# Kernel tuning notes

Measured on AMD Instinct MI355X. Metric: run time of the kernel, lower is better.

## Reference

```python
import jax, jax.numpy as jnp
import numpy as np

B, D_IN, D_OUT = 8192, 4096, 4096
IN_DIMS = (64, 64)
OUT_DIMS = (64, 64)
# tt_rank_rate=0.5 over dims [64,64,64,64] -> ranks [1,32,1024,32,1]
RANKS = (1, 32, 1024, 32, 1)


def _kaiming_uniform(key, shape):
    # matches nn.init.kaiming_uniform_(a=sqrt(5)) on a (r_prev, d, r) tensor:
    # fan_in = prod(shape[1:]) = d * r, gain = sqrt(2/(1+5)) = sqrt(1/3)
    fan_in = shape[1] * shape[2]
    bound = np.sqrt(1.0 / 3.0) * np.sqrt(3.0 / fan_in)
    return jax.random.uniform(key, shape, jnp.float32, -bound, bound)


def setup_inputs() -> dict:
    key = jax.random.key(0)
    kx, k0, k1, k2, k3, kb = jax.random.split(key, 6)
    dims = list(IN_DIMS) + list(OUT_DIMS)
    shapes = [(RANKS[i], dims[i], RANKS[i + 1]) for i in range(4)]
    x = jax.random.normal(kx, (B, D_IN), jnp.float32)
    core0 = _kaiming_uniform(k0, shapes[0])  # (1, 64, 32)
    core1 = _kaiming_uniform(k1, shapes[1])  # (32, 64, 1024)
    core2 = _kaiming_uniform(k2, shapes[2])  # (1024, 64, 32)
    core3 = _kaiming_uniform(k3, shapes[3])  # (32, 64, 1)
    bb = 1.0 / np.sqrt(D_IN)
    bias = jax.random.uniform(kb, (D_OUT,), jnp.float32, -bb, bb)
    return {"x": x, "core0": core0, "core1": core1, "core2": core2,
            "core3": core3, "bias": bias}


def reference(x, core0, core1, core2, core3, bias):
    b = x.shape[0]
    s = x.reshape(b, IN_DIMS[0], IN_DIMS[1])          # (B, 64, 64)
    # input core 0: contract first input dim (rank-in = 1 squeezed)
    s = jnp.einsum('bcd,cs->bds', s, core0[0])        # (B, 64, 32)
    # input core 1: contract second input dim and rank
    s = jnp.einsum('bcr,rcs->bs', s, core1)           # (B, 1024)
    # output core 2: expand first output dim
    s = jnp.einsum('br,rAs->bAs', s, core2)           # (B, 64, 32)
    # output core 3: expand second output dim (rank-out = 1 squeezed)
    s = jnp.einsum('bAr,rB->bAB', s, core3[..., 0])   # (B, 64, 64)
    return s.reshape(b, -1) + bias                    # (B, 4096)
```

## Files before the change

kernel.cpp:

```cpp
#include <hip/hip_runtime.h>
#include <hip/hip_bf16.h>


typedef _Float16 h4 __attribute__((ext_vector_type(4)));
typedef _Float16 h8 __attribute__((ext_vector_type(8)));
typedef float f32x4 __attribute__((ext_vector_type(4)));

#define BATCH 8192

__device__ __forceinline__ void gld_lds16(const void* g, void* l) {
  __builtin_amdgcn_global_load_lds(
      (__attribute__((address_space(1))) void*)(g),
      (__attribute__((address_space(3))) void*)(l), 16, 0, 0);
}

__global__ __launch_bounds__(256) void transpose_cast2(
    const float* __restrict__ c1, _Float16* __restrict__ W1t,
    const float* __restrict__ c2, _Float16* __restrict__ W2t) {
  __shared__ float t[64][65];
  const int which = blockIdx.z;
  const float* src = which ? c2 : c1;
  _Float16* dst = which ? W2t : W1t;
  const int K = which ? 1024 : 2048, U = which ? 2048 : 1024;
  const int k0 = (which ? blockIdx.y : blockIdx.x) * 64;
  const int u0 = (which ? blockIdx.x : blockIdx.y) * 64;
  const int tx = threadIdx.x & 63, ty = threadIdx.x >> 6;
  for (int i = ty; i < 64; i += 4) {
    const int k = k0 + i;
    const int sr = which ? k : ((k & 31) * 64 + (k >> 5));
    t[i][tx] = src[(size_t)sr * U + u0 + tx];
  }
  __syncthreads();
  for (int i = ty; i < 64; i += 4) {
    dst[(size_t)(u0 + i) * K + k0 + tx] = (_Float16)t[tx][i];
  }
}

__global__ __launch_bounds__(256) void stage2(const float* __restrict__ x,
                                              const float* __restrict__ c0,
                                              _Float16* __restrict__ s1) {
  __shared__ _Float16 xh[4 * 4096];
  __shared__ float c0l[2048];
  const int b0 = blockIdx.x * 4;
  const int tid = threadIdx.x;

  {
    const float4* xg = (const float4*)(x + (size_t)b0 * 4096);
#pragma unroll
    for (int k = 0; k < 16; ++k) {
      float4 v = xg[tid + 256 * k];
      h4 w = {(_Float16)v.x, (_Float16)v.y, (_Float16)v.z, (_Float16)v.w};
      ((h4*)xh)[tid + 256 * k] = w;
    }
    ((float4*)c0l)[tid] = ((const float4*)c0)[tid];
    ((float4*)c0l)[tid + 256] = ((const float4*)c0)[tid + 256];
  }
  __syncthreads();

  const int row = tid >> 6, t6 = tid & 63;
  const int d0 = (t6 >> 3) * 8;
  const int r0 = (t6 & 7) * 4;
  const _Float16* xrow = xh + row * 4096;

  float acc[8][4];
#pragma unroll
  for (int i = 0; i < 8; ++i)
#pragma unroll
    for (int j = 0; j < 4; ++j) acc[i][j] = 0.0f;

  for (int c = 0; c < 64; ++c) {
    h8 xv = *(const h8*)&xrow[c * 64 + d0];
    f32x4 wv = *(const f32x4*)&c0l[c * 32 + r0];
#pragma unroll
    for (int i = 0; i < 8; ++i) {
      const float xf = (float)xv[i];
#pragma unroll
      for (int j = 0; j < 4; ++j) acc[i][j] += xf * wv[j];
    }
  }

  _Float16* s1row = s1 + (size_t)(b0 + row) * 2048;
#pragma unroll
  for (int i = 0; i < 8; ++i) {
    h4 o = {(_Float16)acc[i][0], (_Float16)acc[i][1], (_Float16)acc[i][2],
            (_Float16)acc[i][3]};
    *(h4*)&s1row[(d0 + i) * 32 + r0] = o;
  }
}

template <int K, int CN, bool FUSED>
__global__ __launch_bounds__(512, 2) void gemm_pipe(
    const _Float16* __restrict__ A, const _Float16* __restrict__ Bt,
    _Float16* __restrict__ C, const float* __restrict__ c3,
    const float* __restrict__ bias, float* __restrict__ out) {
  __shared__ __align__(16) char lds[3 * 49152];
  constexpr int NT = K / 64;
  const int bm = blockIdx.x, bn = blockIdx.y;
  const int tid = threadIdx.x;
  const int w = tid >> 6, lane = tid & 63;
  const int lr = lane & 15, kh = lane >> 4;
  const int wmo = (w >> 2) << 6, wno = (w & 3) << 6;

  f32x4 acc[4][4] = {};

  const int sr = tid >> 3;
  const int sc = ((tid & 7) ^ (sr & 7)) << 4;
  const char* gA = (const char*)(A + (size_t)(bm * 128 + sr) * K) + sc;
  const char* gB = (const char*)(Bt + (size_t)(bn * 256 + sr) * K) + sc;
  const size_t rk = (size_t)K * 128;
  char* lw = lds + (w << 10);

  auto STAGE = [&](int t) {
    char* b_ = lw + (t % 3) * 49152;
    const char* ga = gA + (size_t)t * 128;
    const char* gb = gB + (size_t)t * 128;
    gld_lds16(ga, b_);
    gld_lds16(ga + rk, b_ + 8192);
    gld_lds16(gb, b_ + 16384);
    gld_lds16(gb + rk, b_ + 24576);
    gld_lds16(gb + 2 * rk, b_ + 32768);
    gld_lds16(gb + 3 * rk, b_ + 40960);
  };

  auto KSTEP = [&](int t) {
    const char* bufA = lds + (t % 3) * 49152;
    const char* bufB = bufA + 16384;
    h8 af[2][4], bf[2][4];
#pragma unroll
    for (int kk = 0; kk < 2; ++kk) {
#pragma unroll
      for (int m = 0; m < 4; ++m) {
        const int R = wmo + m * 16 + lr;
        af[kk][m] = *(const h8*)(bufA + R * 128 +
                                 ((((kk << 2) + kh) ^ (R & 7)) << 4));
      }
#pragma unroll
      for (int n = 0; n < 4; ++n) {
        const int R = wno + n * 16 + lr;
        bf[kk][n] = *(const h8*)(bufB + R * 128 +
                                 ((((kk << 2) + kh) ^ (R & 7)) << 4));
      }
    }
    asm volatile("s_waitcnt lgkmcnt(0)" ::: "memory");
    __builtin_amdgcn_sched_barrier(0);
    __builtin_amdgcn_s_setprio(1);
#pragma unroll
    for (int kk = 0; kk < 2; ++kk)
#pragma unroll
      for (int m = 0; m < 4; ++m)
#pragma unroll
        for (int n = 0; n < 4; ++n)
          acc[m][n] = __builtin_amdgcn_mfma_f32_16x16x32_f16(
              af[kk][m], bf[kk][n], acc[m][n], 0, 0, 0);
    __builtin_amdgcn_s_setprio(0);
    __builtin_amdgcn_sched_barrier(0);
  };

  STAGE(0);
  STAGE(1);
  for (int t = 0; t < NT - 1; ++t) {
    asm volatile("s_waitcnt vmcnt(6)" ::: "memory");
    __builtin_amdgcn_s_barrier();
    __builtin_amdgcn_sched_barrier(0);
    if (t < NT - 2) STAGE(t + 2);
    KSTEP(t);
  }
  asm volatile("s_waitcnt vmcnt(0)" ::: "memory");
  __builtin_amdgcn_s_barrier();
  __builtin_amdgcn_sched_barrier(0);
  KSTEP(NT - 1);

  if constexpr (!FUSED) {
#pragma unroll
    for (int m = 0; m < 4; ++m) {
      const int r0 = bm * 128 + wmo + m * 16 + kh * 4;
#pragma unroll
      for (int n = 0; n < 4; ++n) {
        const int c0 = bn * 256 + wno + n * 16 + lr;
#pragma unroll
        for (int q = 0; q < 4; ++q)
          C[(size_t)(r0 + q) * CN + c0] = (_Float16)acc[m][n][q];
      }
    }
  } else {
    h8 bfe[4];
    float bb[8][4];
#pragma unroll
    for (int n = 0; n < 4; ++n) {
#pragma unroll
      for (int j = 0; j < 8; ++j)
        bfe[n][j] = (_Float16)c3[(kh * 8 + j) * 64 + n * 16 + lr];
#pragma unroll
      for (int a = 0; a < 8; ++a)
        bb[a][n] = bias[(bn * 8 + a) * 64 + n * 16 + lr];
    }
    __syncthreads();
#pragma unroll
    for (int m = 0; m < 4; ++m) {
      const int Rb = wmo + m * 16 + kh * 4;
#pragma unroll
      for (int n = 0; n < 4; ++n) {
        const int cc = wno + n * 16 + lr;
#pragma unroll
        for (int q = 0; q < 4; ++q) {
          const int R = Rb + q;
          *(_Float16*)(lds + R * 512 +
                       ((((cc >> 3) ^ (R & 7)) << 4) | ((cc & 7) << 1))) =
              (_Float16)acc[m][n][q];
        }
      }
    }
    __syncthreads();
    const int row = (w << 4) + lr;
    const int orow0 = bm * 128 + (w << 4) + (kh << 2);
#pragma unroll
    for (int a = 0; a < 8; ++a) {
      h8 afv = *(const h8*)(lds + row * 512 +
                            ((((a << 2) + kh) ^ (row & 7)) << 4));
#pragma unroll
      for (int n = 0; n < 4; ++n) {
        f32x4 d = {};
        d = __builtin_amdgcn_mfma_f32_16x16x32_f16(afv, bfe[n], d, 0, 0, 0);
        const int ocol = (bn * 8 + a) * 64 + n * 16 + lr;
#pragma unroll
        for (int q = 0; q < 4; ++q)
          out[(size_t)(orow0 + q) * 4096 + ocol] = d[q] + bb[a][n];
      }
    }
  }
}

extern "C" void kernel_launch(void* const* d_in, const int* in_sizes, int n_in,
                              void* d_out, int out_size, void* d_ws,
                              size_t ws_size, hipStream_t stream) {
  (void)in_sizes; (void)n_in; (void)out_size; (void)ws_size;
  const float* x     = (const float*)d_in[0];
  const float* core0 = (const float*)d_in[1];
  const float* core1 = (const float*)d_in[2];
  const float* core2 = (const float*)d_in[3];
  const float* core3 = (const float*)d_in[4];
  const float* bias  = (const float*)d_in[5];
  float* out = (float*)d_out;

  char* ws = (char*)d_ws;
  _Float16* s1h = (_Float16*)ws;
  _Float16* s2h = (_Float16*)(ws + 33554432);
  _Float16* W1t = (_Float16*)(ws + 50331648);
  _Float16* W2t = (_Float16*)(ws + 54525952);

  transpose_cast2<<<dim3(32, 16, 2), 256, 0, stream>>>(core1, W1t, core2, W2t);
  stage2<<<BATCH / 4, 256, 0, stream>>>(x, core0, s1h);
  gemm_pipe<2048, 1024, false><<<dim3(BATCH / 128, 4), 512, 0, stream>>>(
      s1h, W1t, s2h, nullptr, nullptr, nullptr);
  gemm_pipe<1024, 4096, true><<<dim3(BATCH / 128, 8), 512, 0, stream>>>(
      s2h, W2t, nullptr, core3, bias, out);
}
```

Before: 155.5 us.

## Split GEMM k-step into two halves interleaving prefetch with MFMA

```diff
diff --git a/kernel.cpp b/kernel.cpp
--- a/kernel.cpp
+++ b/kernel.cpp
@@ -110,19 +110,28 @@
   const size_t rk = (size_t)K * 128;
   char* lw = lds + (w << 10);
 
-  auto STAGE = [&](int t) {
+  auto STAGE_A = [&](int t) {
     char* b_ = lw + (t % 3) * 49152;
     const char* ga = gA + (size_t)t * 128;
-    const char* gb = gB + (size_t)t * 128;
     gld_lds16(ga, b_);
     gld_lds16(ga + rk, b_ + 8192);
-    gld_lds16(gb, b_ + 16384);
+    gld_lds16(gB + (size_t)t * 128, b_ + 16384);
+  };
+  auto STAGE_B = [&](int t) {
+    char* b_ = lw + (t % 3) * 49152;
+    const char* gb = gB + (size_t)t * 128;
     gld_lds16(gb + rk, b_ + 24576);
     gld_lds16(gb + 2 * rk, b_ + 32768);
     gld_lds16(gb + 3 * rk, b_ + 40960);
   };
 
-  auto KSTEP = [&](int t) {
+  auto KTILE = [&](int t, bool last) {
+    if (last)
+      asm volatile("s_waitcnt vmcnt(0)" ::: "memory");
+    else
+      asm volatile("s_waitcnt vmcnt(6)" ::: "memory");
+    __builtin_amdgcn_s_barrier();
+    __builtin_amdgcn_sched_barrier(0);
     const char* bufA = lds + (t % 3) * 49152;
     const char* bufB = bufA + 16384;
     h8 af[2][4], bf[2][4];
@@ -135,12 +144,13 @@
                                  ((((kk << 2) + kh) ^ (R & 7)) << 4));
       }
 #pragma unroll
-      for (int n = 0; n < 4; ++n) {
+      for (int n = 0; n < 2; ++n) {
         const int R = wno + n * 16 + lr;
         bf[kk][n] = *(const h8*)(bufB + R * 128 +
                                  ((((kk << 2) + kh) ^ (R & 7)) << 4));
       }
     }
+    if (t + 2 < NT) STAGE_A(t + 2);
     asm volatile("s_waitcnt lgkmcnt(0)" ::: "memory");
     __builtin_amdgcn_sched_barrier(0);
     __builtin_amdgcn_s_setprio(1);
@@ -149,26 +159,39 @@
 #pragma unroll
       for (int m = 0; m < 4; ++m)
 #pragma unroll
-        for (int n = 0; n < 4; ++n)
+        for (int n = 0; n < 2; ++n)
           acc[m][n] = __builtin_amdgcn_mfma_f32_16x16x32_f16(
               af[kk][m], bf[kk][n], acc[m][n], 0, 0, 0);
     __builtin_amdgcn_s_setprio(0);
-    __builtin_amdgcn_sched_barrier(0);
+    __builtin_amdgcn_s_barrier();
+    __builtin_amdgcn_sched_barrier(0);
+#pragma unroll
+    for (int kk = 0; kk < 2; ++kk)
+#pragma unroll
+      for (int n = 2; n < 4; ++n) {
+        const int R = wno + n * 16 + lr;
+        bf[kk][n] = *(const h8*)(bufB + R * 128 +
+                                 ((((kk << 2) + kh) ^ (R & 7)) << 4));
+      }
+    if (t + 2 < NT) STAGE_B(t + 2);
+    asm volatile("s_waitcnt lgkmcnt(0)" ::: "memory");
+    __builtin_amdgcn_sched_barrier(0);
+    __builtin_amdgcn_s_setprio(1);
+#pragma unroll
+    for (int kk = 0; kk < 2; ++kk)
+#pragma unroll
+      for (int m = 0; m < 4; ++m)
+#pragma unroll
+        for (int n = 2; n < 4; ++n)
+          acc[m][n] = __builtin_amdgcn_mfma_f32_16x16x32_f16(
+              af[kk][m], bf[kk][n], acc[m][n], 0, 0, 0);
+    __builtin_amdgcn_s_setprio(0);
   };
 
-  STAGE(0);
-  STAGE(1);
-  for (int t = 0; t < NT - 1; ++t) {
-    asm volatile("s_waitcnt vmcnt(6)" ::: "memory");
-    __builtin_amdgcn_s_barrier();
-    __builtin_amdgcn_sched_barrier(0);
-    if (t < NT - 2) STAGE(t + 2);
-    KSTEP(t);
-  }
-  asm volatile("s_waitcnt vmcnt(0)" ::: "memory");
-  __builtin_amdgcn_s_barrier();
-  __builtin_amdgcn_sched_barrier(0);
-  KSTEP(NT - 1);
+  STAGE_A(0); STAGE_B(0);
+  STAGE_A(1); STAGE_B(1);
+  for (int t = 0; t < NT - 1; ++t) KTILE(t, false);
+  KTILE(NT - 1, true);
 
   if constexpr (!FUSED) {
 #pragma unroll
```

New measurement: 151.6 us. 1.03x faster.
